# Optimization experiments

Hardware: AMD Instinct MI355X
Metric: run time of the kernel (lower is better)

## Reference

```python
import jax, jax.numpy as jnp
import numpy as np

N_LAYERS = 4
EPS = 1e-5  # eqx.nn.LayerNorm default


def _kernels(lam, P, B, C, step, L):
    # Annotated-S4 DPLR generating-function kernel (Q = P), vectorized over H channels.
    # lam, P, B, C: (H, N) complex64; step: (H, 1) real. Returns K: (H, L) real.
    omega = jnp.exp((-2j * jnp.pi) * (jnp.arange(L) / L))            # (L,) roots of unity
    g = (2.0 / step) * ((1.0 - omega) / (1.0 + omega))[None, :]      # (H, L) bilinear warp
    c = 2.0 / (1.0 + omega)                                          # (L,)

    def cauchy(v):  # v: (H, N) -> (H, L): sum_n v_n / (g - lambda_n)
        return jnp.sum(v[:, None, :] / (g[:, :, None] - lam[:, None, :]), axis=-1)

    k00 = cauchy(jnp.conj(C) * B)
    k01 = cauchy(jnp.conj(C) * P)
    k10 = cauchy(jnp.conj(P) * B)
    k11 = cauchy(jnp.conj(P) * P)
    at_roots = c[None, :] * (k00 - k01 * (1.0 / (1.0 + k11)) * k10)  # woodbury correction
    return jnp.fft.ifft(at_roots, n=L, axis=-1).real                 # (H, L)


def _causal_conv(u, K):
    # u: (B, L, H) real input, K: (H, L) real kernel -> causal conv along L via zero-padded FFT.
    L = u.shape[1]
    Ud = jnp.fft.rfft(u, n=2 * L, axis=1)                 # (B, F, H)
    Kd = jnp.fft.rfft(K, n=2 * L, axis=-1)                # (H, F)
    return jnp.fft.irfft(Ud * Kd.T[None], n=2 * L, axis=1)[:, :L]


def _forward(x, enc_w, enc_b, dec_w, dec_b, lam_re, lam_im, p_re, p_im, b_re, b_im,
             c_re, c_im, d, log_step, norm_w, norm_b, w1, b1, w2, b2):
    L = x.shape[1]
    h = x @ enc_w.T + enc_b                               # encoder: (B, L, H)
    for i in range(N_LAYERS):
        skip = h
        mu = h.mean(-1, keepdims=True)
        var = ((h - mu) ** 2).mean(-1, keepdims=True)
        hn = (h - mu) / jnp.sqrt(var + EPS) * norm_w[i] + norm_b[i]
        K = _kernels(lam_re[i] + 1j * lam_im[i], p_re[i] + 1j * p_im[i],
                     b_re[i] + 1j * b_im[i], c_re[i] + 1j * c_im[i],
                     jnp.exp(log_step[i])[:, None], L)
        y = _causal_conv(hn, K) + hn * d[i]               # SSM conv + skip-through D term
        y = jax.nn.gelu(y)
        y = (y @ w1[i].T + b1[i]) * jax.nn.sigmoid(y @ w2[i].T + b2[i])  # gated MLP
        h = skip + y
    return h @ dec_w.T + dec_b                            # decoder: (B, L, out)


def setup_inputs() -> dict:
    key = jax.random.key(0)
    B, L, IN, OUT, H, N, NL = 8, 2048, 64, 64, 128, 64, N_LAYERS
    ks = jax.random.split(key, 12)
    rn = lambda k, s, sc: (jax.random.normal(k, s) * sc).astype(jnp.float32)
    return dict(
        x=rn(ks[0], (B, L, IN), 1.0),
        convolve=1,
        enc_w=rn(ks[1], (H, IN), 1.0 / np.sqrt(IN)), enc_b=jnp.zeros((H,), jnp.float32),
        dec_w=rn(ks[2], (OUT, H), 1.0 / np.sqrt(H)), dec_b=jnp.zeros((OUT,), jnp.float32),
        lam_re=-0.5 * jnp.ones((NL, H, N), jnp.float32),  # HiPPO/S4D-style stable poles
        lam_im=jnp.tile(jnp.float32(np.pi) * jnp.arange(N, dtype=jnp.float32), (NL, H, 1)),
        p_re=rn(ks[3], (NL, H, N), 0.5 / np.sqrt(N)), p_im=rn(ks[4], (NL, H, N), 0.5 / np.sqrt(N)),
        b_re=rn(ks[5], (NL, H, N), 1.0), b_im=rn(ks[6], (NL, H, N), 1.0),
        c_re=rn(ks[7], (NL, H, N), 1.0 / np.sqrt(N)), c_im=rn(ks[8], (NL, H, N), 1.0 / np.sqrt(N)),
        d=jnp.ones((NL, H), jnp.float32),
        log_step=(jax.random.uniform(ks[9], (NL, H)) * (np.log(0.1) - np.log(0.001))
                  + np.log(0.001)).astype(jnp.float32),
        norm_w=jnp.ones((NL, H), jnp.float32), norm_b=jnp.zeros((NL, H), jnp.float32),
        w1=rn(ks[10], (NL, H, H), 1.0 / np.sqrt(H)), b1=jnp.zeros((NL, H), jnp.float32),
        w2=rn(ks[11], (NL, H, H), 1.0 / np.sqrt(H)), b2=jnp.zeros((NL, H), jnp.float32),
    )


def reference(x, convolve, enc_w, enc_b, dec_w, dec_b, lam_re, lam_im, p_re, p_im,
              b_re, b_im, c_re, c_im, d, log_step, norm_w, norm_b, w1, b1, w2, b2):
    # convolve is static 1 (True): the FFT-convolution path of the S4 Model.
    return _forward(x, enc_w, enc_b, dec_w, dec_b, lam_re, lam_im, p_re, p_im, b_re, b_im,
                    c_re, c_im, d, log_step, norm_w, norm_b, w1, b1, w2, b2)
```

## Files before the change

### kernel.cpp

```cpp
#include <hip/hip_runtime.h>
#include <hip/hip_bf16.h>


#define Bsz 8
#define Lseq 2048
#define Hdim 128
#define Npol 64
#define NLAYERS 4

typedef __bf16 bf16x8 __attribute__((ext_vector_type(8)));
typedef float f32x16 __attribute__((ext_vector_type(16)));

__device__ __forceinline__ float fast_rcp(float x) { return __builtin_amdgcn_rcpf(x); }
__device__ __forceinline__ float fast_rsq(float x) { return __builtin_amdgcn_rsqf(x); }

__device__ __forceinline__ float2 cmulf(float2 a, float2 b) {
    return make_float2(a.x * b.x - a.y * b.y, a.x * b.y + a.y * b.x);
}
__device__ __forceinline__ float2 cmulc(float2 a, float2 b) {
    return make_float2(a.x * b.x + a.y * b.y, a.y * b.x - a.x * b.y);
}

__device__ __forceinline__ float gelu_f(float v) {
    float z = 0.7978845608028654f * (v + 0.044715f * v * v * v);
    float e = __expf(2.0f * z);
    return v - v * fast_rcp(e + 1.0f);
}

__device__ __forceinline__ int sw(int i) { return (i & ~15) | ((i ^ (i >> 4)) & 15); }

static __device__ const float W16R[8] = {1.f, 0.9238795325f, 0.7071067812f, 0.3826834324f,
                                         0.f, -0.3826834324f, -0.7071067812f, -0.9238795325f};
static __device__ const float W16I[8] = {0.f, -0.3826834324f, -0.7071067812f, -0.9238795325f,
                                         -1.f, -0.9238795325f, -0.7071067812f, -0.3826834324f};
static __device__ const int BR4[16] = {0, 8, 4, 12, 2, 10, 6, 14, 1, 9, 5, 13, 3, 11, 7, 15};
static __device__ const int BR3[8] = {0, 4, 2, 6, 1, 5, 3, 7};

__device__ __forceinline__ float2 twget(const float2* __restrict__ tw, int e) {
    float2 w = tw[e & 2047];
    if (e & 2048) { w.x = -w.x; w.y = -w.y; }
    return w;
}

template <bool INV>
__device__ __forceinline__ void fft16_dif(float2 v[16]) {
#pragma unroll
    for (int mi = 0; mi < 4; mi++) {
        const int m = 8 >> mi;
#pragma unroll
        for (int g = 0; g < 16; g += 2 * m) {
#pragma unroll
            for (int j = 0; j < m; j++) {
                float wr = W16R[j << mi];
                float wi = INV ? -W16I[j << mi] : W16I[j << mi];
                float2 a = v[g + j], b = v[g + j + m];
                float dx = a.x - b.x, dy = a.y - b.y;
                v[g + j] = make_float2(a.x + b.x, a.y + b.y);
                v[g + j + m] = make_float2(dx * wr - dy * wi, dx * wi + dy * wr);
            }
        }
    }
}

template <bool INV>
__device__ __forceinline__ void fft16_dit(float2 v[16]) {
#pragma unroll
    for (int mi = 3; mi >= 0; mi--) {
        const int m = 8 >> mi;
#pragma unroll
        for (int g = 0; g < 16; g += 2 * m) {
#pragma unroll
            for (int j = 0; j < m; j++) {
                float wr = W16R[j << mi];
                float wi = INV ? -W16I[j << mi] : W16I[j << mi];
                float2 a = v[g + j], b = v[g + j + m];
                float bx = b.x * wr - b.y * wi, by = b.x * wi + b.y * wr;
                v[g + j] = make_float2(a.x + bx, a.y + by);
                v[g + j + m] = make_float2(a.x - bx, a.y - by);
            }
        }
    }
}

template <bool INV>
__device__ __forceinline__ void fft8_dif(float2 v[8]) {
#pragma unroll
    for (int mi = 0; mi < 3; mi++) {
        const int m = 4 >> mi;
#pragma unroll
        for (int g = 0; g < 8; g += 2 * m) {
#pragma unroll
            for (int j = 0; j < m; j++) {
                float wr = W16R[j << (mi + 1)];
                float wi = INV ? -W16I[j << (mi + 1)] : W16I[j << (mi + 1)];
                float2 a = v[g + j], b = v[g + j + m];
                float dx = a.x - b.x, dy = a.y - b.y;
                v[g + j] = make_float2(a.x + b.x, a.y + b.y);
                v[g + j + m] = make_float2(dx * wr - dy * wi, dx * wi + dy * wr);
            }
        }
    }
}

__device__ __forceinline__ void fft4096_passA_hz(float2* data, const float2* __restrict__ tw,
                                                 int t, const float2 vin[8]) {
    float2 v[16];
#pragma unroll
    for (int j = 0; j < 8; j++) v[j] = vin[j];
#pragma unroll
    for (int j = 0; j < 8; j++)
        v[j + 8] = cmulf(v[j], make_float2(W16R[j], W16I[j]));
#pragma unroll
    for (int mi = 1; mi < 4; mi++) {
        const int m = 8 >> mi;
#pragma unroll
        for (int g = 0; g < 16; g += 2 * m) {
#pragma unroll
            for (int j = 0; j < m; j++) {
                float wr = W16R[j << mi], wi = W16I[j << mi];
                float2 a = v[g + j], b = v[g + j + m];
                float dx = a.x - b.x, dy = a.y - b.y;
                v[g + j] = make_float2(a.x + b.x, a.y + b.y);
                v[g + j + m] = make_float2(dx * wr - dy * wi, dx * wi + dy * wr);
            }
        }
    }
#pragma unroll
    for (int i = 1; i < 16; i++) v[i] = cmulf(v[i], twget(tw, t * BR4[i]));
#pragma unroll
    for (int i = 0; i < 16; i++) data[sw(i * 256 + t)] = v[i];
}

__device__ __forceinline__ void fft4096_fwd_BC(float2* data, const float2* __restrict__ tw, int t) {
    __syncthreads();
    {
        int j0 = t & 15;
        int base = (t >> 4) * 256 + j0;
        float2 v[16];
#pragma unroll
        for (int k = 0; k < 16; k++) v[k] = data[sw(base + 16 * k)];
        fft16_dif<false>(v);
#pragma unroll
        for (int i = 1; i < 16; i++) v[i] = cmulf(v[i], twget(tw, 16 * j0 * BR4[i]));
#pragma unroll
        for (int i = 0; i < 16; i++) data[sw(base + 16 * i)] = v[i];
    }
    __syncthreads();
    {
        float2 v[16];
#pragma unroll
        for (int k = 0; k < 16; k++) v[k] = data[sw(t * 16 + k)];
        fft16_dif<false>(v);
#pragma unroll
        for (int i = 0; i < 16; i++) data[sw(t * 16 + i)] = v[i];
    }
    __syncthreads();
}

__device__ __forceinline__ void kfft_core(int hh, int t, float* smem,
                                          float2* __restrict__ KdL,
                                          const float2* __restrict__ tw,
                                          const float* __restrict__ lam_re,
                                          const float* __restrict__ lam_im,
                                          const float* __restrict__ p_re,
                                          const float* __restrict__ p_im,
                                          const float* __restrict__ b_re,
                                          const float* __restrict__ b_im,
                                          const float* __restrict__ c_re,
                                          const float* __restrict__ c_im,
                                          const float* __restrict__ log_step) {
    float2* data = (float2*)smem;
    float4* polA = (float4*)(smem + 8192);
    float4* polB = (float4*)(smem + 8448);
    float* n11S = smem + 8704;
    float* ktmp = smem + 8192;
    int baseP = hh * Npol;
    if (t < Npol) {
        int n = t;
        float lr = lam_re[baseP + n], li = lam_im[baseP + n];
        float pr = p_re[baseP + n], pi = p_im[baseP + n];
        float br = b_re[baseP + n], bi = b_im[baseP + n];
        float cr = c_re[baseP + n], ci = c_im[baseP + n];
        polA[n] = make_float4(lr, li, cr * br + ci * bi, cr * bi - ci * br);
        polB[n] = make_float4(cr * pr + ci * pi, cr * pi - ci * pr,
                              pr * br + pi * bi, pr * bi - pi * br);
        n11S[n] = pr * pr + pi * pi;
    }
    __syncthreads();
    {
        float step = expf(log_step[hh]);
        float gs = 2.0f / step;
        float wrv[8], wiv[8];
        float gr[8], gi[8];
#pragma unroll
        for (int j = 0; j < 8; j++) {
            int l = t + 256 * j;
            float ang = -6.283185307179586f * (float)l / (float)Lseq;
            float wr = cosf(ang), wi = sinf(ang);
            wrv[j] = wr; wiv[j] = wi;
            float dr = 1.0f + wr, di = wi;
            float invd2 = fast_rcp(dr * dr + di * di);
            float nr = 1.0f - wr, ni = -wi;
            gr[j] = gs * (nr * dr + ni * di) * invd2;
            gi[j] = gs * (ni * dr - nr * di) * invd2;
        }
        float k00x[8], k00y[8], k01x[8], k01y[8];
        float k10x[8], k10y[8], k11x[8], k11y[8];
#pragma unroll
        for (int j = 0; j < 8; j++) {
            k00x[j] = 0.f; k00y[j] = 0.f; k01x[j] = 0.f; k01y[j] = 0.f;
            k10x[j] = 0.f; k10y[j] = 0.f; k11x[j] = 0.f; k11y[j] = 0.f;
        }
        for (int n = 0; n < Npol; n++) {
            float4 A = polA[n];
            float4 B = polB[n];
            float n11 = n11S[n];
#pragma unroll
            for (int j = 0; j < 8; j++) {
                float er = gr[j] - A.x, ei = gi[j] - A.y;
                float inv2 = fast_rcp(fmaf(er, er, ei * ei));
                float ir = er * inv2;
                float mi = ei * inv2;
                k00x[j] = fmaf(A.z, ir, fmaf(A.w, mi, k00x[j]));
                k00y[j] = fmaf(A.w, ir, fmaf(-A.z, mi, k00y[j]));
                k01x[j] = fmaf(B.x, ir, fmaf(B.y, mi, k01x[j]));
                k01y[j] = fmaf(B.y, ir, fmaf(-B.x, mi, k01y[j]));
                k10x[j] = fmaf(B.z, ir, fmaf(B.w, mi, k10x[j]));
                k10y[j] = fmaf(B.w, ir, fmaf(-B.z, mi, k10y[j]));
                k11x[j] = fmaf(n11, ir, k11x[j]);
                k11y[j] = fmaf(-n11, mi, k11y[j]);
            }
        }
#pragma unroll
        for (int j = 0; j < 8; j++) {
            int l = t + 256 * j;
            float dr = 1.0f + wrv[j], di = wiv[j];
            float invd2 = fast_rcp(dr * dr + di * di);
            float cr2 = 2.0f * dr * invd2, ci2 = -2.0f * di * invd2;
            float wr2 = 1.0f + k11x[j], wi2 = k11y[j];
            float w2inv = fast_rcp(fmaf(wr2, wr2, wi2 * wi2));
            float vr = wr2 * w2inv, vi = -wi2 * w2inv;
            float t1x = k01x[j] * k10x[j] - k01y[j] * k10y[j];
            float t1y = k01x[j] * k10y[j] + k01y[j] * k10x[j];
            float t2x = t1x * vr - t1y * vi, t2y = t1x * vi + t1y * vr;
            float ex = k00x[j] - t2x, ey = k00y[j] - t2y;
            data[sw(l)] = make_float2(cr2 * ex - ci2 * ey, cr2 * ey + ci2 * ex);
        }
    }
    __syncthreads();
    if (t < 128) {
        float2 v[16];
#pragma unroll
        for (int k = 0; k < 16; k++) v[k] = data[sw(t + 128 * k)];
        fft16_dif<true>(v);
#pragma unroll
        for (int i = 1; i < 16; i++) v[i] = cmulc(v[i], twget(tw, 2 * t * BR4[i]));
#pragma unroll
        for (int i = 0; i < 16; i++) data[sw(i * 128 + t)] = v[i];
    }
    __syncthreads();
    if (t < 128) {
        int i2 = t >> 3, j0 = t & 7;
        int base2 = i2 * 128 + j0;
        float2 v[16];
#pragma unroll
        for (int k = 0; k < 16; k++) v[k] = data[sw(base2 + 8 * k)];
        fft16_dif<true>(v);
#pragma unroll
        for (int i = 1; i < 16; i++) v[i] = cmulc(v[i], twget(tw, 32 * j0 * BR4[i]));
#pragma unroll
        for (int i = 0; i < 16; i++) data[sw(base2 + 8 * i)] = v[i];
    }
    __syncthreads();
    {
        float2 v8[8];
#pragma unroll
        for (int k = 0; k < 8; k++) v8[k] = data[sw(t * 8 + k)];
        fft8_dif<true>(v8);
        int r = BR4[t >> 4], s = BR4[t & 15];
#pragma unroll
        for (int i = 0; i < 8; i++) {
            int l = r + 16 * s + 256 * BR3[i];
            ktmp[l] = v8[i].x * (1.0f / 2048.0f);
        }
    }
    __syncthreads();
    {
        float2 vin[8];
#pragma unroll
        for (int k = 0; k < 8; k++) vin[k] = make_float2(ktmp[t + 256 * k], 0.f);
        fft4096_passA_hz(data, tw, t, vin);
    }
    fft4096_fwd_BC(data, tw, t);
    float2* dst = KdL + (size_t)hh * 4096;
#pragma unroll
    for (int k = 0; k < 16; k++) {
        int p = t + 256 * k;
        dst[p] = data[sw(p)];
    }
}

__global__ __launch_bounds__(256, 4) void prep_kernel(const float* __restrict__ w1,
                                                      const float* __restrict__ w2,
                                                      const float* __restrict__ dec_w,
                                                      const float* __restrict__ enc_w,
                                                      float2* __restrict__ tw,
                                                      __bf16* __restrict__ wbf,
                                                      __bf16* __restrict__ decbf,
                                                      __bf16* __restrict__ encbf) {
    int bid = blockIdx.x, t = threadIdx.x;
    if (bid < 8) {
        int k = bid * 256 + t;
        if (k < 2048) {
            double a = -6.283185307179586476925286766559 * (double)k / 4096.0;
            tw[k] = make_float2((float)cos(a), (float)sin(a));
        }
        return;
    }
    if (bid < 264) {
        int i = (bid - 8) * 256 + t;
        int layer = i >> 14, rem = i & 16383;
        wbf[((size_t)layer * 2) * 16384 + rem] = (__bf16)w1[i];
        wbf[((size_t)layer * 2 + 1) * 16384 + rem] = (__bf16)w2[i];
        return;
    }
    if (bid < 296) {
        int i = (bid - 264) * 256 + t;
        decbf[i] = (__bf16)dec_w[i];
        return;
    }
    int i = (bid - 296) * 256 + t;
    encbf[i] = (__bf16)enc_w[i];
}

__global__ __launch_bounds__(256) void kfft_enc_kernel(float2* __restrict__ Kd1,
                                                       const float2* __restrict__ tw,
                                                       const float* __restrict__ x,
                                                       const __bf16* __restrict__ encbf,
                                                       const float* __restrict__ enc_b,
                                                       const float* __restrict__ nw,
                                                       const float* __restrict__ nb,
                                                       float* __restrict__ h,
                                                       float* __restrict__ hnT,
                                                       const float* __restrict__ lam_re,
                                                       const float* __restrict__ lam_im,
                                                       const float* __restrict__ p_re,
                                                       const float* __restrict__ p_im,
                                                       const float* __restrict__ b_re,
                                                       const float* __restrict__ b_im,
                                                       const float* __restrict__ c_re,
                                                       const float* __restrict__ c_im,
                                                       const float* __restrict__ log_step) {
    __shared__ __align__(16) float smem[10240];
    int bid = blockIdx.x, t = threadIdx.x;
    if (bid < 512) {
        int hh = bid & 127, layer = bid >> 7;
        int PN = Hdim * Npol;
        kfft_core(hh, t, smem, Kd1 + (size_t)layer * Hdim * 4096, tw,
                  lam_re + layer * PN, lam_im + layer * PN,
                  p_re + layer * PN, p_im + layer * PN,
                  b_re + layer * PN, b_im + layer * PN,
                  c_re + layer * PN, c_im + layer * PN,
                  log_step + layer * Hdim);
    } else {
        int r0 = (bid - 512) * 32;
        __bf16* ybf = (__bf16*)smem;
        float* dots = smem + 1152;
        float2* mv = (float2*)(smem + 5376);
        int bb = r0 >> 11, l0 = r0 & 2047;
        for (int i = t; i < 32 * 64; i += 256) {
            int r = i >> 6, k = i & 63;
            ybf[r * 72 + k] = (__bf16)x[(size_t)(r0 + r) * 64 + k];
        }
        __syncthreads();
        int wave = t >> 6, lane = t & 63;
        int m = lane & 31, half = lane >> 5;
        bf16x8 a[4];
#pragma unroll
        for (int kk = 0; kk < 4; kk++)
            a[kk] = *(const bf16x8*)&ybf[m * 72 + kk * 16 + half * 8];
        int o = 32 * wave + m;
        const __bf16* wr = encbf + (size_t)o * 64 + half * 8;
        f32x16 acc;
#pragma unroll
        for (int i = 0; i < 16; i++) acc[i] = 0.f;
#pragma unroll
        for (int kk = 0; kk < 4; kk++) {
            bf16x8 bw = *(const bf16x8*)(wr + kk * 16);
            acc = __builtin_amdgcn_mfma_f32_32x32x16_bf16(a[kk], bw, acc, 0, 0, 0);
        }
        float bo = enc_b[o];
#pragma unroll
        for (int reg = 0; reg < 16; reg++) {
            int row = (reg & 3) + 8 * (reg >> 2) + 4 * half;
            dots[row * 132 + o] = acc[reg] + bo;
        }
        __syncthreads();
        {
            int row = t >> 3, lane8 = t & 7;
            float s1 = 0.f, s2 = 0.f;
            int base = row * 132 + lane8 * 16;
#pragma unroll
            for (int q = 0; q < 4; q++) {
                float4 v4 = *(const float4*)&dots[base + 4 * q];
                s1 += v4.x + v4.y + v4.z + v4.w;
                s2 += v4.x * v4.x + v4.y * v4.y + v4.z * v4.z + v4.w * v4.w;
            }
#pragma unroll
            for (int mm = 1; mm < 8; mm <<= 1) { s1 += __shfl_xor(s1, mm); s2 += __shfl_xor(s2, mm); }
            if (lane8 == 0) {
                float mu = s1 * (1.0f / 128.0f);
                float var = s2 * (1.0f / 128.0f) - mu * mu;
                mv[row] = make_float2(mu, fast_rsq(var + 1e-5f));
            }
        }
        __syncthreads();
        {
            int o2 = t & 127, rh = t >> 7;
            float nwc = nw[o2], nbc = nb[o2];
            float hnv[16];
#pragma unroll
            for (int j = 0; j < 16; j++) {
                int r = rh * 16 + j;
                float hvv = dots[r * 132 + o2];
                h[(size_t)(r0 + r) * Hdim + o2] = hvv;
                float2 mvv = mv[r];
                hnv[j] = (hvv - mvv.x) * mvv.y * nwc + nbc;
            }
            float* dst = hnT + ((size_t)bb * Hdim + o2) * Lseq + l0 + rh * 16;
            *(float4*)(dst)      = make_float4(hnv[0],  hnv[1],  hnv[2],  hnv[3]);
            *(float4*)(dst + 4)  = make_float4(hnv[4],  hnv[5],  hnv[6],  hnv[7]);
            *(float4*)(dst + 8)  = make_float4(hnv[8],  hnv[9],  hnv[10], hnv[11]);
            *(float4*)(dst + 12) = make_float4(hnv[12], hnv[13], hnv[14], hnv[15]);
        }
    }
}

__global__ __launch_bounds__(256) void conv_kernel(float* __restrict__ hnT,
                                                   const float2* __restrict__ Kd1,
                                                   const float* __restrict__ dvec,
                                                   const float2* __restrict__ tw) {
    int h = blockIdx.x, bp = blockIdx.y, t = threadIdx.x;
    __shared__ float2 data[4096];
    float* u0 = hnT + ((size_t)(2 * bp) * Hdim + h) * Lseq;
    float* u1 = hnT + ((size_t)(2 * bp + 1) * Hdim + h) * Lseq;
    float2 ureg[8];
    float2 Kreg[16];
    float2 twB[15];
    const int j0 = t & 15;
    const float4* Kp4 = (const float4*)(Kd1 + (size_t)h * 4096 + t * 16);
    {
        float2 vin[8];
#pragma unroll
        for (int k = 0; k < 8; k++) {
            int l = t + 256 * k;
            float2 u2 = make_float2(u0[l], u1[l]);
            ureg[k] = u2;
            vin[k] = u2;
        }
#pragma unroll
        for (int k = 0; k < 8; k++) {
            float4 q = Kp4[k];
            Kreg[2 * k]     = make_float2(q.x, q.y);
            Kreg[2 * k + 1] = make_float2(q.z, q.w);
        }
#pragma unroll
        for (int i = 1; i < 16; i++) twB[i - 1] = twget(tw, 16 * j0 * BR4[i]);
        fft4096_passA_hz(data, tw, t, vin);
    }
    __syncthreads();
    {
        int base = (t >> 4) * 256 + j0;
        float2 v[16];
#pragma unroll
        for (int k = 0; k < 16; k++) v[k] = data[sw(base + 16 * k)];
        fft16_dif<false>(v);
#pragma unroll
        for (int i = 1; i < 16; i++) v[i] = cmulf(v[i], twB[i - 1]);
#pragma unroll
        for (int i = 0; i < 16; i++) data[sw(base + 16 * i)] = v[i];
    }
    __syncthreads();
    {
        const float scale = 1.0f / 4096.0f;
        float2 v[16];
#pragma unroll
        for (int k = 0; k < 16; k++) v[k] = data[sw(t * 16 + k)];
        fft16_dif<false>(v);
#pragma unroll
        for (int i = 0; i < 16; i++) {
            float2 W = cmulf(v[i], Kreg[i]);
            v[i] = make_float2(W.x * scale, W.y * scale);
        }
        fft16_dit<true>(v);
#pragma unroll
        for (int i = 0; i < 16; i++) data[sw(t * 16 + i)] = v[i];
    }
    __syncthreads();
    {
        int base2 = (t >> 4) * 256 + j0;
        float2 v[16];
        v[0] = data[sw(base2)];
#pragma unroll
        for (int i = 1; i < 16; i++)
            v[i] = cmulc(data[sw(base2 + 16 * i)], twB[i - 1]);
        fft16_dit<true>(v);
#pragma unroll
        for (int i = 0; i < 16; i++) data[sw(base2 + 16 * i)] = v[i];
    }
    __syncthreads();
    {
        float2 v[16];
        v[0] = data[sw(t)];
#pragma unroll
        for (int i = 1; i < 16; i++)
            v[i] = cmulc(data[sw(i * 256 + t)], twget(tw, t * BR4[i]));
#pragma unroll
        for (int mi = 3; mi >= 1; mi--) {
            const int m = 8 >> mi;
#pragma unroll
            for (int g = 0; g < 16; g += 2 * m) {
#pragma unroll
                for (int j = 0; j < m; j++) {
                    float wr = W16R[j << mi], wi = -W16I[j << mi];
                    float2 a = v[g + j], bb2 = v[g + j + m];
                    float bx = bb2.x * wr - bb2.y * wi, by = bb2.x * wi + bb2.y * wr;
                    v[g + j] = make_float2(a.x + bx, a.y + by);
                    v[g + j + m] = make_float2(a.x - bx, a.y - by);
                }
            }
        }
#pragma unroll
        for (int j = 0; j < 8; j++) {
            float wr = W16R[j], wi = -W16I[j];
            float2 bb2 = v[j + 8];
            float bx = bb2.x * wr - bb2.y * wi, by = bb2.x * wi + bb2.y * wr;
            v[j] = make_float2(v[j].x + bx, v[j].y + by);
        }
        float dcoef = dvec[h];
#pragma unroll
        for (int k = 0; k < 8; k++) {
            int l = t + 256 * k;
            u0[l] = gelu_f(v[k].x + ureg[k].x * dcoef);
            u1[l] = gelu_f(v[k].y + ureg[k].y * dcoef);
        }
    }
}

__global__ __launch_bounds__(256) void mlp_kernel(const float* __restrict__ yT,
                                                  float* __restrict__ h,
                                                  float* __restrict__ hnT,
                                                  const __bf16* __restrict__ w1b,
                                                  const __bf16* __restrict__ w2b,
                                                  const float* __restrict__ b1,
                                                  const float* __restrict__ b2,
                                                  const float* __restrict__ nw,
                                                  const float* __restrict__ nb) {
    int r0 = blockIdx.x * 32;
    int t = threadIdx.x;
    int wave = t >> 6, lane = t & 63;
    __shared__ __align__(16) __bf16 ybf[32 * 136];
    __shared__ float dots[32 * 132];
    __shared__ float2 mv[32];
    int bb = r0 >> 11, l0 = r0 & 2047;
    for (int i = t; i < 32 * 128; i += 256) {
        int r = i & 31, k = i >> 5;
        ybf[r * 136 + k] = (__bf16)yT[((size_t)bb * Hdim + k) * Lseq + l0 + r];
    }
    __syncthreads();
    int m = lane & 31, half = lane >> 5;
    bf16x8 a[8];
#pragma unroll
    for (int kk = 0; kk < 8; kk++)
        a[kk] = *(const bf16x8*)&ybf[m * 136 + kk * 16 + half * 8];
    int out = 32 * wave + m;
    const __bf16* w1r = w1b + (size_t)out * 128 + half * 8;
    const __bf16* w2r = w2b + (size_t)out * 128 + half * 8;
    f32x16 acc1, acc2;
#pragma unroll
    for (int i = 0; i < 16; i++) { acc1[i] = 0.f; acc2[i] = 0.f; }
#pragma unroll
    for (int kk = 0; kk < 8; kk++) {
        bf16x8 bw1 = *(const bf16x8*)(w1r + kk * 16);
        bf16x8 bw2 = *(const bf16x8*)(w2r + kk * 16);
        acc1 = __builtin_amdgcn_mfma_f32_32x32x16_bf16(a[kk], bw1, acc1, 0, 0, 0);
        acc2 = __builtin_amdgcn_mfma_f32_32x32x16_bf16(a[kk], bw2, acc2, 0, 0, 0);
    }
    float bias1 = b1[out], bias2 = b2[out];
#pragma unroll
    for (int reg = 0; reg < 16; reg++) {
        int row = (reg & 3) + 8 * (reg >> 2) + 4 * half;
        float v1 = acc1[reg] + bias1;
        float v2 = acc2[reg] + bias2;
        float g = fast_rcp(1.0f + __expf(-v2));
        float hv = h[(size_t)(r0 + row) * Hdim + out] + v1 * g;
        dots[row * 132 + out] = hv;
    }
    __syncthreads();
    {
        int row = t >> 3, lane8 = t & 7;
        float s1 = 0.f, s2 = 0.f;
        int base = row * 132 + lane8 * 16;
#pragma unroll
        for (int q = 0; q < 4; q++) {
            float4 v4 = *(const float4*)&dots[base + 4 * q];
            s1 += v4.x + v4.y + v4.z + v4.w;
            s2 += v4.x * v4.x + v4.y * v4.y + v4.z * v4.z + v4.w * v4.w;
        }
#pragma unroll
        for (int mm = 1; mm < 8; mm <<= 1) { s1 += __shfl_xor(s1, mm); s2 += __shfl_xor(s2, mm); }
        if (lane8 == 0) {
            float mu = s1 * (1.0f / 128.0f);
            float var = s2 * (1.0f / 128.0f) - mu * mu;
            mv[row] = make_float2(mu, fast_rsq(var + 1e-5f));
        }
    }
    __syncthreads();
    {
        int o = t & 127, rh = t >> 7;
        float nwc = nw[o], nbc = nb[o];
        float hnv[16];
#pragma unroll
        for (int j = 0; j < 16; j++) {
            int r = rh * 16 + j;
            float hvv = dots[r * 132 + o];
            h[(size_t)(r0 + r) * Hdim + o] = hvv;
            float2 mvv = mv[r];
            hnv[j] = (hvv - mvv.x) * mvv.y * nwc + nbc;
        }
        float* dst = hnT + ((size_t)bb * Hdim + o) * Lseq + l0 + rh * 16;
        *(float4*)(dst)      = make_float4(hnv[0],  hnv[1],  hnv[2],  hnv[3]);
        *(float4*)(dst + 4)  = make_float4(hnv[4],  hnv[5],  hnv[6],  hnv[7]);
        *(float4*)(dst + 8)  = make_float4(hnv[8],  hnv[9],  hnv[10], hnv[11]);
        *(float4*)(dst + 12) = make_float4(hnv[12], hnv[13], hnv[14], hnv[15]);
    }
}

__global__ __launch_bounds__(256) void mlpdec_kernel(const float* __restrict__ yT,
                                                     const float* __restrict__ h,
                                                     const __bf16* __restrict__ w1b,
                                                     const __bf16* __restrict__ w2b,
                                                     const float* __restrict__ b1,
                                                     const float* __restrict__ b2,
                                                     const __bf16* __restrict__ decb,
                                                     const float* __restrict__ dec_bias,
                                                     float* __restrict__ out) {
    int r0 = blockIdx.x * 32;
    int t = threadIdx.x;
    int wave = t >> 6, lane = t & 63;
    __shared__ __align__(16) __bf16 ybf[32 * 136];
    __shared__ float dots[32 * 132];
    int bb = r0 >> 11, l0 = r0 & 2047;
    for (int i = t; i < 32 * 128; i += 256) {
        int r = i & 31, k = i >> 5;
        ybf[r * 136 + k] = (__bf16)yT[((size_t)bb * Hdim + k) * Lseq + l0 + r];
    }
    __syncthreads();
    int m = lane & 31, half = lane >> 5;
    bf16x8 a[8];
#pragma unroll
    for (int kk = 0; kk < 8; kk++)
        a[kk] = *(const bf16x8*)&ybf[m * 136 + kk * 16 + half * 8];
    int outc = 32 * wave + m;
    const __bf16* w1r = w1b + (size_t)outc * 128 + half * 8;
    const __bf16* w2r = w2b + (size_t)outc * 128 + half * 8;
    f32x16 acc1, acc2;
#pragma unroll
    for (int i = 0; i < 16; i++) { acc1[i] = 0.f; acc2[i] = 0.f; }
#pragma unroll
    for (int kk = 0; kk < 8; kk++) {
        bf16x8 bw1 = *(const bf16x8*)(w1r + kk * 16);
        bf16x8 bw2 = *(const bf16x8*)(w2r + kk * 16);
        acc1 = __builtin_amdgcn_mfma_f32_32x32x16_bf16(a[kk], bw1, acc1, 0, 0, 0);
        acc2 = __builtin_amdgcn_mfma_f32_32x32x16_bf16(a[kk], bw2, acc2, 0, 0, 0);
    }
    float bias1 = b1[outc], bias2 = b2[outc];
#pragma unroll
    for (int reg = 0; reg < 16; reg++) {
        int row = (reg & 3) + 8 * (reg >> 2) + 4 * half;
        float v1 = acc1[reg] + bias1;
        float v2 = acc2[reg] + bias2;
        float g = fast_rcp(1.0f + __expf(-v2));
        float hv = h[(size_t)(r0 + row) * Hdim + outc] + v1 * g;
        dots[row * 132 + outc] = hv;
    }
    __syncthreads();
    for (int i = t; i < 32 * 128; i += 256) {
        int r = i >> 7, k = i & 127;
        ybf[r * 136 + k] = (__bf16)dots[r * 132 + k];
    }
    __syncthreads();
    if (wave < 2) {
        bf16x8 a2[8];
#pragma unroll
        for (int kk = 0; kk < 8; kk++)
            a2[kk] = *(const bf16x8*)&ybf[m * 136 + kk * 16 + half * 8];
        int oc = 32 * wave + m;
        const __bf16* wr = decb + (size_t)oc * 128 + half * 8;
        f32x16 acc;
#pragma unroll
        for (int i = 0; i < 16; i++) acc[i] = 0.f;
#pragma unroll
        for (int kk = 0; kk < 8; kk++) {
            bf16x8 bw = *(const bf16x8*)(wr + kk * 16);
            acc = __builtin_amdgcn_mfma_f32_32x32x16_bf16(a2[kk], bw, acc, 0, 0, 0);
        }
        float bo = dec_bias[oc];
#pragma unroll
        for (int reg = 0; reg < 16; reg++) {
            int row = (reg & 3) + 8 * (reg >> 2) + 4 * half;
            out[(size_t)(r0 + row) * 64 + oc] = acc[reg] + bo;
        }
    }
}

extern "C" void kernel_launch(void* const* d_in, const int* in_sizes, int n_in,
                              void* d_out, int out_size, void* d_ws, size_t ws_size,
                              hipStream_t stream) {
    const float* x      = (const float*)d_in[0];
    const float* enc_w  = (const float*)d_in[2];
    const float* enc_b  = (const float*)d_in[3];
    const float* dec_w  = (const float*)d_in[4];
    const float* dec_b  = (const float*)d_in[5];
    const float* lam_re = (const float*)d_in[6];
    const float* lam_im = (const float*)d_in[7];
    const float* p_re   = (const float*)d_in[8];
    const float* p_im   = (const float*)d_in[9];
    const float* b_re   = (const float*)d_in[10];
    const float* b_im   = (const float*)d_in[11];
    const float* c_re   = (const float*)d_in[12];
    const float* c_im   = (const float*)d_in[13];
    const float* dvec   = (const float*)d_in[14];
    const float* lstep  = (const float*)d_in[15];
    const float* norm_w = (const float*)d_in[16];
    const float* norm_b = (const float*)d_in[17];
    const float* w1     = (const float*)d_in[18];
    const float* b1     = (const float*)d_in[19];
    const float* w2     = (const float*)d_in[20];
    const float* b2     = (const float*)d_in[21];
    float* out = (float*)d_out;

    char* ws = (char*)d_ws;
    float2* tw  = (float2*)ws;  ws += 2048 * sizeof(float2);
    float*  h   = (float*)ws;   ws += (size_t)Bsz * Lseq * Hdim * sizeof(float);
    float*  hnT = (float*)ws;   ws += (size_t)Bsz * Lseq * Hdim * sizeof(float);
    float2* Kd1 = (float2*)ws;  ws += (size_t)NLAYERS * Hdim * 4096 * sizeof(float2);
    __bf16* wbf = (__bf16*)ws;  ws += (size_t)NLAYERS * 2 * Hdim * Hdim * sizeof(__bf16);
    __bf16* dbf = (__bf16*)ws;  ws += (size_t)64 * Hdim * sizeof(__bf16);
    __bf16* ebf = (__bf16*)ws;  ws += (size_t)Hdim * 64 * sizeof(__bf16);

    const int nrows = Bsz * Lseq;

    prep_kernel<<<328, 256, 0, stream>>>(w1, w2, dec_w, enc_w, tw, wbf, dbf, ebf);
    kfft_enc_kernel<<<512 + nrows / 32, 256, 0, stream>>>(
        Kd1, tw, x, ebf, enc_b, norm_w, norm_b, h, hnT,
        lam_re, lam_im, p_re, p_im, b_re, b_im, c_re, c_im, lstep);
    for (int L = 0; L < NLAYERS; L++) {
        conv_kernel<<<dim3(Hdim, Bsz / 2), 256, 0, stream>>>(
            hnT, Kd1 + (size_t)L * Hdim * 4096, dvec + L * Hdim, tw);
        const __bf16* w1bL = wbf + (size_t)L * 2 * Hdim * Hdim;
        const __bf16* w2bL = w1bL + Hdim * Hdim;
        if (L < NLAYERS - 1) {
            const float* nwn = norm_w + (L + 1) * Hdim;
            const float* nbn = norm_b + (L + 1) * Hdim;
            mlp_kernel<<<nrows / 32, 256, 0, stream>>>(hnT, h, hnT, w1bL, w2bL,
                                                       b1 + L * Hdim, b2 + L * Hdim,
                                                       nwn, nbn);
        } else {
            mlpdec_kernel<<<nrows / 32, 256, 0, stream>>>(hnT, h, w1bL, w2bL,
                                                          b1 + L * Hdim, b2 + L * Hdim,
                                                          dbf, dec_b, out);
        }
    }
}
```

Measured before the change: 277.5 us.

## Write conv output as bf16 to separate buffer and widen kfft blocks to 512 threads

The conv kernel now writes the GELU output as bf16 into a new buffer instead of overwriting hnT in fp32, and the MLP kernels read bf16 directly. This halves the write and read traffic of the intermediate activation between conv and MLP. Separately, the kernel-generation/encoder kernel is launched with 512 threads, splitting the Cauchy sum over 4 instead of 8 points per thread, while the FFT and encoder phases stay on 256 threads with the rest idle. The wider block adds more barriers and idle threads in the FFT/encoder sections.

```diff
diff --git a/kernel.cpp b/kernel.cpp
--- a/kernel.cpp
+++ b/kernel.cpp
@@ -131,173 +131,25 @@
     for (int i = 0; i < 16; i++) data[sw(i * 256 + t)] = v[i];
 }
 
-__device__ __forceinline__ void fft4096_fwd_BC(float2* data, const float2* __restrict__ tw, int t) {
-    __syncthreads();
-    {
-        int j0 = t & 15;
-        int base = (t >> 4) * 256 + j0;
-        float2 v[16];
-#pragma unroll
-        for (int k = 0; k < 16; k++) v[k] = data[sw(base + 16 * k)];
-        fft16_dif<false>(v);
-#pragma unroll
-        for (int i = 1; i < 16; i++) v[i] = cmulf(v[i], twget(tw, 16 * j0 * BR4[i]));
-#pragma unroll
-        for (int i = 0; i < 16; i++) data[sw(base + 16 * i)] = v[i];
-    }
-    __syncthreads();
-    {
-        float2 v[16];
-#pragma unroll
-        for (int k = 0; k < 16; k++) v[k] = data[sw(t * 16 + k)];
-        fft16_dif<false>(v);
-#pragma unroll
-        for (int i = 0; i < 16; i++) data[sw(t * 16 + i)] = v[i];
-    }
-    __syncthreads();
-}
-
-__device__ __forceinline__ void kfft_core(int hh, int t, float* smem,
-                                          float2* __restrict__ KdL,
-                                          const float2* __restrict__ tw,
-                                          const float* __restrict__ lam_re,
-                                          const float* __restrict__ lam_im,
-                                          const float* __restrict__ p_re,
-                                          const float* __restrict__ p_im,
-                                          const float* __restrict__ b_re,
-                                          const float* __restrict__ b_im,
-                                          const float* __restrict__ c_re,
-                                          const float* __restrict__ c_im,
-                                          const float* __restrict__ log_step) {
-    float2* data = (float2*)smem;
-    float4* polA = (float4*)(smem + 8192);
-    float4* polB = (float4*)(smem + 8448);
-    float* n11S = smem + 8704;
-    float* ktmp = smem + 8192;
-    int baseP = hh * Npol;
-    if (t < Npol) {
-        int n = t;
-        float lr = lam_re[baseP + n], li = lam_im[baseP + n];
-        float pr = p_re[baseP + n], pi = p_im[baseP + n];
-        float br = b_re[baseP + n], bi = b_im[baseP + n];
-        float cr = c_re[baseP + n], ci = c_im[baseP + n];
-        polA[n] = make_float4(lr, li, cr * br + ci * bi, cr * bi - ci * br);
-        polB[n] = make_float4(cr * pr + ci * pi, cr * pi - ci * pr,
-                              pr * br + pi * bi, pr * bi - pi * br);
-        n11S[n] = pr * pr + pi * pi;
-    }
-    __syncthreads();
-    {
-        float step = expf(log_step[hh]);
-        float gs = 2.0f / step;
-        float wrv[8], wiv[8];
-        float gr[8], gi[8];
-#pragma unroll
-        for (int j = 0; j < 8; j++) {
-            int l = t + 256 * j;
-            float ang = -6.283185307179586f * (float)l / (float)Lseq;
-            float wr = cosf(ang), wi = sinf(ang);
-            wrv[j] = wr; wiv[j] = wi;
-            float dr = 1.0f + wr, di = wi;
-            float invd2 = fast_rcp(dr * dr + di * di);
-            float nr = 1.0f - wr, ni = -wi;
-            gr[j] = gs * (nr * dr + ni * di) * invd2;
-            gi[j] = gs * (ni * dr - nr * di) * invd2;
-        }
-        float k00x[8], k00y[8], k01x[8], k01y[8];
-        float k10x[8], k10y[8], k11x[8], k11y[8];
-#pragma unroll
-        for (int j = 0; j < 8; j++) {
-            k00x[j] = 0.f; k00y[j] = 0.f; k01x[j] = 0.f; k01y[j] = 0.f;
-            k10x[j] = 0.f; k10y[j] = 0.f; k11x[j] = 0.f; k11y[j] = 0.f;
-        }
-        for (int n = 0; n < Npol; n++) {
-            float4 A = polA[n];
-            float4 B = polB[n];
-            float n11 = n11S[n];
-#pragma unroll
-            for (int j = 0; j < 8; j++) {
-                float er = gr[j] - A.x, ei = gi[j] - A.y;
-                float inv2 = fast_rcp(fmaf(er, er, ei * ei));
-                float ir = er * inv2;
-                float mi = ei * inv2;
-                k00x[j] = fmaf(A.z, ir, fmaf(A.w, mi, k00x[j]));
-                k00y[j] = fmaf(A.w, ir, fmaf(-A.z, mi, k00y[j]));
-                k01x[j] = fmaf(B.x, ir, fmaf(B.y, mi, k01x[j]));
-                k01y[j] = fmaf(B.y, ir, fmaf(-B.x, mi, k01y[j]));
-                k10x[j] = fmaf(B.z, ir, fmaf(B.w, mi, k10x[j]));
-                k10y[j] = fmaf(B.w, ir, fmaf(-B.z, mi, k10y[j]));
-                k11x[j] = fmaf(n11, ir, k11x[j]);
-                k11y[j] = fmaf(-n11, mi, k11y[j]);
-            }
-        }
-#pragma unroll
-        for (int j = 0; j < 8; j++) {
-            int l = t + 256 * j;
-            float dr = 1.0f + wrv[j], di = wiv[j];
-            float invd2 = fast_rcp(dr * dr + di * di);
-            float cr2 = 2.0f * dr * invd2, ci2 = -2.0f * di * invd2;
-            float wr2 = 1.0f + k11x[j], wi2 = k11y[j];
-            float w2inv = fast_rcp(fmaf(wr2, wr2, wi2 * wi2));
-            float vr = wr2 * w2inv, vi = -wi2 * w2inv;
-            float t1x = k01x[j] * k10x[j] - k01y[j] * k10y[j];
-            float t1y = k01x[j] * k10y[j] + k01y[j] * k10x[j];
-            float t2x = t1x * vr - t1y * vi, t2y = t1x * vi + t1y * vr;
-            float ex = k00x[j] - t2x, ey = k00y[j] - t2y;
-            data[sw(l)] = make_float2(cr2 * ex - ci2 * ey, cr2 * ey + ci2 * ex);
-        }
-    }
-    __syncthreads();
-    if (t < 128) {
-        float2 v[16];
-#pragma unroll
-        for (int k = 0; k < 16; k++) v[k] = data[sw(t + 128 * k)];
-        fft16_dif<true>(v);
-#pragma unroll
-        for (int i = 1; i < 16; i++) v[i] = cmulc(v[i], twget(tw, 2 * t * BR4[i]));
-#pragma unroll
-        for (int i = 0; i < 16; i++) data[sw(i * 128 + t)] = v[i];
-    }
-    __syncthreads();
-    if (t < 128) {
-        int i2 = t >> 3, j0 = t & 7;
-        int base2 = i2 * 128 + j0;
-        float2 v[16];
-#pragma unroll
-        for (int k = 0; k < 16; k++) v[k] = data[sw(base2 + 8 * k)];
-        fft16_dif<true>(v);
-#pragma unroll
-        for (int i = 1; i < 16; i++) v[i] = cmulc(v[i], twget(tw, 32 * j0 * BR4[i]));
-#pragma unroll
-        for (int i = 0; i < 16; i++) data[sw(base2 + 8 * i)] = v[i];
-    }
-    __syncthreads();
-    {
-        float2 v8[8];
-#pragma unroll
-        for (int k = 0; k < 8; k++) v8[k] = data[sw(t * 8 + k)];
-        fft8_dif<true>(v8);
-        int r = BR4[t >> 4], s = BR4[t & 15];
-#pragma unroll
-        for (int i = 0; i < 8; i++) {
-            int l = r + 16 * s + 256 * BR3[i];
-            ktmp[l] = v8[i].x * (1.0f / 2048.0f);
-        }
-    }
-    __syncthreads();
-    {
-        float2 vin[8];
-#pragma unroll
-        for (int k = 0; k < 8; k++) vin[k] = make_float2(ktmp[t + 256 * k], 0.f);
-        fft4096_passA_hz(data, tw, t, vin);
-    }
-    fft4096_fwd_BC(data, tw, t);
-    float2* dst = KdL + (size_t)hh * 4096;
-#pragma unroll
-    for (int k = 0; k < 16; k++) {
-        int p = t + 256 * k;
-        dst[p] = data[sw(p)];
-    }
+__device__ __forceinline__ void fft4096_fwd_B(float2* data, const float2* __restrict__ tw, int t) {
+    int j0 = t & 15;
+    int base = (t >> 4) * 256 + j0;
+    float2 v[16];
+#pragma unroll
+    for (int k = 0; k < 16; k++) v[k] = data[sw(base + 16 * k)];
+    fft16_dif<false>(v);
+#pragma unroll
+    for (int i = 1; i < 16; i++) v[i] = cmulf(v[i], twget(tw, 16 * j0 * BR4[i]));
+#pragma unroll
+    for (int i = 0; i < 16; i++) data[sw(base + 16 * i)] = v[i];
+}
+__device__ __forceinline__ void fft4096_fwd_C(float2* data, int t) {
+    float2 v[16];
+#pragma unroll
+    for (int k = 0; k < 16; k++) v[k] = data[sw(t * 16 + k)];
+    fft16_dif<false>(v);
+#pragma unroll
+    for (int i = 0; i < 16; i++) data[sw(t * 16 + i)] = v[i];
 }
 
 __global__ __launch_bounds__(256, 4) void prep_kernel(const float* __restrict__ w1,
@@ -333,7 +185,7 @@
     encbf[i] = (__bf16)enc_w[i];
 }
 
-__global__ __launch_bounds__(256) void kfft_enc_kernel(float2* __restrict__ Kd1,
+__global__ __launch_bounds__(512) void kfft_enc_kernel(float2* __restrict__ Kd1,
                                                        const float2* __restrict__ tw,
                                                        const float* __restrict__ x,
                                                        const __bf16* __restrict__ encbf,
@@ -356,47 +208,184 @@
     if (bid < 512) {
         int hh = bid & 127, layer = bid >> 7;
         int PN = Hdim * Npol;
-        kfft_core(hh, t, smem, Kd1 + (size_t)layer * Hdim * 4096, tw,
-                  lam_re + layer * PN, lam_im + layer * PN,
-                  p_re + layer * PN, p_im + layer * PN,
-                  b_re + layer * PN, b_im + layer * PN,
-                  c_re + layer * PN, c_im + layer * PN,
-                  log_step + layer * Hdim);
+        const float* lre = lam_re + layer * PN;
+        const float* lim = lam_im + layer * PN;
+        const float* pre = p_re + layer * PN;
+        const float* pim = p_im + layer * PN;
+        const float* bre = b_re + layer * PN;
+        const float* bim = b_im + layer * PN;
+        const float* cre = c_re + layer * PN;
+        const float* cim = c_im + layer * PN;
+        const float* lst = log_step + layer * Hdim;
+        float2* data = (float2*)smem;
+        float4* polA = (float4*)(smem + 8192);
+        float4* polB = (float4*)(smem + 8448);
+        float* n11S = smem + 8704;
+        float* ktmp = smem + 8192;
+        int baseP = hh * Npol;
+        if (t < Npol) {
+            int n = t;
+            float lr = lre[baseP + n], li = lim[baseP + n];
+            float pr = pre[baseP + n], pi = pim[baseP + n];
+            float br = bre[baseP + n], bi = bim[baseP + n];
+            float cr = cre[baseP + n], ci = cim[baseP + n];
+            polA[n] = make_float4(lr, li, cr * br + ci * bi, cr * bi - ci * br);
+            polB[n] = make_float4(cr * pr + ci * pi, cr * pi - ci * pr,
+                                  pr * br + pi * bi, pr * bi - pi * br);
+            n11S[n] = pr * pr + pi * pi;
+        }
+        __syncthreads();
+        {
+            float step = expf(lst[hh]);
+            float gs = 2.0f / step;
+            float wrv[4], wiv[4], gr[4], gi[4];
+#pragma unroll
+            for (int j = 0; j < 4; j++) {
+                int l = t + 512 * j;
+                float ang = -6.283185307179586f * (float)l / (float)Lseq;
+                float wr = cosf(ang), wi = sinf(ang);
+                wrv[j] = wr; wiv[j] = wi;
+                float dr = 1.0f + wr, di = wi;
+                float invd2 = fast_rcp(dr * dr + di * di);
+                float nr = 1.0f - wr, ni = -wi;
+                gr[j] = gs * (nr * dr + ni * di) * invd2;
+                gi[j] = gs * (ni * dr - nr * di) * invd2;
+            }
+            float k00x[4], k00y[4], k01x[4], k01y[4];
+            float k10x[4], k10y[4], k11x[4], k11y[4];
+#pragma unroll
+            for (int j = 0; j < 4; j++) {
+                k00x[j] = 0.f; k00y[j] = 0.f; k01x[j] = 0.f; k01y[j] = 0.f;
+                k10x[j] = 0.f; k10y[j] = 0.f; k11x[j] = 0.f; k11y[j] = 0.f;
+            }
+            for (int n = 0; n < Npol; n++) {
+                float4 A = polA[n];
+                float4 B = polB[n];
+                float n11 = n11S[n];
+#pragma unroll
+                for (int j = 0; j < 4; j++) {
+                    float er = gr[j] - A.x, ei = gi[j] - A.y;
+                    float inv2 = fast_rcp(fmaf(er, er, ei * ei));
+                    float ir = er * inv2;
+                    float mi = ei * inv2;
+                    k00x[j] = fmaf(A.z, ir, fmaf(A.w, mi, k00x[j]));
+                    k00y[j] = fmaf(A.w, ir, fmaf(-A.z, mi, k00y[j]));
+                    k01x[j] = fmaf(B.x, ir, fmaf(B.y, mi, k01x[j]));
+                    k01y[j] = fmaf(B.y, ir, fmaf(-B.x, mi, k01y[j]));
+                    k10x[j] = fmaf(B.z, ir, fmaf(B.w, mi, k10x[j]));
+                    k10y[j] = fmaf(B.w, ir, fmaf(-B.z, mi, k10y[j]));
+                    k11x[j] = fmaf(n11, ir, k11x[j]);
+                    k11y[j] = fmaf(-n11, mi, k11y[j]);
+                }
+            }
+#pragma unroll
+            for (int j = 0; j < 4; j++) {
+                int l = t + 512 * j;
+                float dr = 1.0f + wrv[j], di = wiv[j];
+                float invd2 = fast_rcp(dr * dr + di * di);
+                float cr2 = 2.0f * dr * invd2, ci2 = -2.0f * di * invd2;
+                float wr2 = 1.0f + k11x[j], wi2 = k11y[j];
+                float w2inv = fast_rcp(fmaf(wr2, wr2, wi2 * wi2));
+                float vr = wr2 * w2inv, vi = -wi2 * w2inv;
+                float t1x = k01x[j] * k10x[j] - k01y[j] * k10y[j];
+                float t1y = k01x[j] * k10y[j] + k01y[j] * k10x[j];
+                float t2x = t1x * vr - t1y * vi, t2y = t1x * vi + t1y * vr;
+                float ex = k00x[j] - t2x, ey = k00y[j] - t2y;
+                data[sw(l)] = make_float2(cr2 * ex - ci2 * ey, cr2 * ey + ci2 * ex);
+            }
+        }
+        __syncthreads();
+        if (t < 128) {
+            float2 v[16];
+#pragma unroll
+            for (int k = 0; k < 16; k++) v[k] = data[sw(t + 128 * k)];
+            fft16_dif<true>(v);
+#pragma unroll
+            for (int i = 1; i < 16; i++) v[i] = cmulc(v[i], twget(tw, 2 * t * BR4[i]));
+#pragma unroll
+            for (int i = 0; i < 16; i++) data[sw(i * 128 + t)] = v[i];
+        }
+        __syncthreads();
+        if (t < 128) {
+            int i2 = t >> 3, j0 = t & 7;
+            int base2 = i2 * 128 + j0;
+            float2 v[16];
+#pragma unroll
+            for (int k = 0; k < 16; k++) v[k] = data[sw(base2 + 8 * k)];
+            fft16_dif<true>(v);
+#pragma unroll
+            for (int i = 1; i < 16; i++) v[i] = cmulc(v[i], twget(tw, 32 * j0 * BR4[i]));
+#pragma unroll
+            for (int i = 0; i < 16; i++) data[sw(base2 + 8 * i)] = v[i];
+        }
+        __syncthreads();
+        if (t < 256) {
+            float2 v8[8];
+#pragma unroll
+            for (int k = 0; k < 8; k++) v8[k] = data[sw(t * 8 + k)];
+            fft8_dif<true>(v8);
+            int r = BR4[t >> 4], s = BR4[t & 15];
+#pragma unroll
+            for (int i = 0; i < 8; i++) {
+                int l = r + 16 * s + 256 * BR3[i];
+                ktmp[l] = v8[i].x * (1.0f / 2048.0f);
+            }
+        }
+        __syncthreads();
+        if (t < 256) {
+            float2 vin[8];
+#pragma unroll
+            for (int k = 0; k < 8; k++) vin[k] = make_float2(ktmp[t + 256 * k], 0.f);
+            fft4096_passA_hz(data, tw, t, vin);
+        }
+        __syncthreads();
+        if (t < 256) fft4096_fwd_B(data, tw, t);
+        __syncthreads();
+        if (t < 256) fft4096_fwd_C(data, t);
+        __syncthreads();
+        float2* dst = Kd1 + ((size_t)layer * Hdim + hh) * 4096;
+#pragma unroll
+        for (int k = 0; k < 8; k++) {
+            int p = t + 512 * k;
+            dst[p] = data[sw(p)];
+        }
     } else {
         int r0 = (bid - 512) * 32;
         __bf16* ybf = (__bf16*)smem;
         float* dots = smem + 1152;
         float2* mv = (float2*)(smem + 5376);
         int bb = r0 >> 11, l0 = r0 & 2047;
-        for (int i = t; i < 32 * 64; i += 256) {
+        for (int i = t; i < 32 * 64; i += 512) {
             int r = i >> 6, k = i & 63;
             ybf[r * 72 + k] = (__bf16)x[(size_t)(r0 + r) * 64 + k];
         }
         __syncthreads();
-        int wave = t >> 6, lane = t & 63;
-        int m = lane & 31, half = lane >> 5;
-        bf16x8 a[4];
-#pragma unroll
-        for (int kk = 0; kk < 4; kk++)
-            a[kk] = *(const bf16x8*)&ybf[m * 72 + kk * 16 + half * 8];
-        int o = 32 * wave + m;
-        const __bf16* wr = encbf + (size_t)o * 64 + half * 8;
-        f32x16 acc;
-#pragma unroll
-        for (int i = 0; i < 16; i++) acc[i] = 0.f;
-#pragma unroll
-        for (int kk = 0; kk < 4; kk++) {
-            bf16x8 bw = *(const bf16x8*)(wr + kk * 16);
-            acc = __builtin_amdgcn_mfma_f32_32x32x16_bf16(a[kk], bw, acc, 0, 0, 0);
-        }
-        float bo = enc_b[o];
-#pragma unroll
-        for (int reg = 0; reg < 16; reg++) {
-            int row = (reg & 3) + 8 * (reg >> 2) + 4 * half;
-            dots[row * 132 + o] = acc[reg] + bo;
-        }
-        __syncthreads();
-        {
+        if (t < 256) {
+            int wave = t >> 6, lane = t & 63;
+            int m = lane & 31, half = lane >> 5;
+            bf16x8 a[4];
+#pragma unroll
+            for (int kk = 0; kk < 4; kk++)
+                a[kk] = *(const bf16x8*)&ybf[m * 72 + kk * 16 + half * 8];
+            int o = 32 * wave + m;
+            const __bf16* wr = encbf + (size_t)o * 64 + half * 8;
+            f32x16 acc;
+#pragma unroll
+            for (int i = 0; i < 16; i++) acc[i] = 0.f;
+#pragma unroll
+            for (int kk = 0; kk < 4; kk++) {
+                bf16x8 bw = *(const bf16x8*)(wr + kk * 16);
+                acc = __builtin_amdgcn_mfma_f32_32x32x16_bf16(a[kk], bw, acc, 0, 0, 0);
+            }
+            float bo = enc_b[o];
+#pragma unroll
+            for (int reg = 0; reg < 16; reg++) {
+                int row = (reg & 3) + 8 * (reg >> 2) + 4 * half;
+                dots[row * 132 + o] = acc[reg] + bo;
+            }
+        }
+        __syncthreads();
+        if (t < 256) {
             int row = t >> 3, lane8 = t & 7;
             float s1 = 0.f, s2 = 0.f;
             int base = row * 132 + lane8 * 16;
@@ -415,7 +404,7 @@
             }
         }
         __syncthreads();
-        {
+        if (t < 256) {
             int o2 = t & 127, rh = t >> 7;
             float nwc = nw[o2], nbc = nb[o2];
             float hnv[16];
@@ -436,14 +425,17 @@
     }
 }
 
-__global__ __launch_bounds__(256) void conv_kernel(float* __restrict__ hnT,
+__global__ __launch_bounds__(256) void conv_kernel(const float* __restrict__ hnT,
+                                                   __bf16* __restrict__ ybuf,
                                                    const float2* __restrict__ Kd1,
                                                    const float* __restrict__ dvec,
                                                    const float2* __restrict__ tw) {
     int h = blockIdx.x, bp = blockIdx.y, t = threadIdx.x;
     __shared__ float2 data[4096];
-    float* u0 = hnT + ((size_t)(2 * bp) * Hdim + h) * Lseq;
-    float* u1 = hnT + ((size_t)(2 * bp + 1) * Hdim + h) * Lseq;
+    const float* u0 = hnT + ((size_t)(2 * bp) * Hdim + h) * Lseq;
+    const float* u1 = hnT + ((size_t)(2 * bp + 1) * Hdim + h) * Lseq;
+    __bf16* y0 = ybuf + ((size_t)(2 * bp) * Hdim + h) * Lseq;
+    __bf16* y1 = ybuf + ((size_t)(2 * bp + 1) * Hdim + h) * Lseq;
     float2 ureg[8];
     float2 Kreg[16];
     float2 twB[15];
@@ -541,13 +533,13 @@
 #pragma unroll
         for (int k = 0; k < 8; k++) {
             int l = t + 256 * k;
-            u0[l] = gelu_f(v[k].x + ureg[k].x * dcoef);
-            u1[l] = gelu_f(v[k].y + ureg[k].y * dcoef);
-        }
-    }
-}
-
-__global__ __launch_bounds__(256) void mlp_kernel(const float* __restrict__ yT,
+            y0[l] = (__bf16)gelu_f(v[k].x + ureg[k].x * dcoef);
+            y1[l] = (__bf16)gelu_f(v[k].y + ureg[k].y * dcoef);
+        }
+    }
+}
+
+__global__ __launch_bounds__(256) void mlp_kernel(const __bf16* __restrict__ yT,
                                                   float* __restrict__ h,
                                                   float* __restrict__ hnT,
                                                   const __bf16* __restrict__ w1b,
@@ -565,7 +557,7 @@
     int bb = r0 >> 11, l0 = r0 & 2047;
     for (int i = t; i < 32 * 128; i += 256) {
         int r = i & 31, k = i >> 5;
-        ybf[r * 136 + k] = (__bf16)yT[((size_t)bb * Hdim + k) * Lseq + l0 + r];
+        ybf[r * 136 + k] = yT[((size_t)bb * Hdim + k) * Lseq + l0 + r];
     }
     __syncthreads();
     int m = lane & 31, half = lane >> 5;
@@ -636,7 +628,7 @@
     }
 }
 
-__global__ __launch_bounds__(256) void mlpdec_kernel(const float* __restrict__ yT,
+__global__ __launch_bounds__(256) void mlpdec_kernel(const __bf16* __restrict__ yT,
                                                      const float* __restrict__ h,
                                                      const __bf16* __restrict__ w1b,
                                                      const __bf16* __restrict__ w2b,
@@ -653,7 +645,7 @@
     int bb = r0 >> 11, l0 = r0 & 2047;
     for (int i = t; i < 32 * 128; i += 256) {
         int r = i & 31, k = i >> 5;
-        ybf[r * 136 + k] = (__bf16)yT[((size_t)bb * Hdim + k) * Lseq + l0 + r];
+        ybf[r * 136 + k] = yT[((size_t)bb * Hdim + k) * Lseq + l0 + r];
     }
     __syncthreads();
     int m = lane & 31, half = lane >> 5;
@@ -744,6 +736,7 @@
     float2* tw  = (float2*)ws;  ws += 2048 * sizeof(float2);
     float*  h   = (float*)ws;   ws += (size_t)Bsz * Lseq * Hdim * sizeof(float);
     float*  hnT = (float*)ws;   ws += (size_t)Bsz * Lseq * Hdim * sizeof(float);
+    __bf16* ybuf = (__bf16*)ws; ws += (size_t)Bsz * Lseq * Hdim * sizeof(__bf16);
     float2* Kd1 = (float2*)ws;  ws += (size_t)NLAYERS * Hdim * 4096 * sizeof(float2);
     __bf16* wbf = (__bf16*)ws;  ws += (size_t)NLAYERS * 2 * Hdim * Hdim * sizeof(__bf16);
     __bf16* dbf = (__bf16*)ws;  ws += (size_t)64 * Hdim * sizeof(__bf16);
@@ -752,22 +745,22 @@
     const int nrows = Bsz * Lseq;
 
     prep_kernel<<<328, 256, 0, stream>>>(w1, w2, dec_w, enc_w, tw, wbf, dbf, ebf);
-    kfft_enc_kernel<<<512 + nrows / 32, 256, 0, stream>>>(
+    kfft_enc_kernel<<<512 + nrows / 32, 512, 0, stream>>>(
         Kd1, tw, x, ebf, enc_b, norm_w, norm_b, h, hnT,
         lam_re, lam_im, p_re, p_im, b_re, b_im, c_re, c_im, lstep);
     for (int L = 0; L < NLAYERS; L++) {
         conv_kernel<<<dim3(Hdim, Bsz / 2), 256, 0, stream>>>(
-            hnT, Kd1 + (size_t)L * Hdim * 4096, dvec + L * Hdim, tw);
+            hnT, ybuf, Kd1 + (size_t)L * Hdim * 4096, dvec + L * Hdim, tw);
         const __bf16* w1bL = wbf + (size_t)L * 2 * Hdim * Hdim;
         const __bf16* w2bL = w1bL + Hdim * Hdim;
         if (L < NLAYERS - 1) {
             const float* nwn = norm_w + (L + 1) * Hdim;
             const float* nbn = norm_b + (L + 1) * Hdim;
-            mlp_kernel<<<nrows / 32, 256, 0, stream>>>(hnT, h, hnT, w1bL, w2bL,
+            mlp_kernel<<<nrows / 32, 256, 0, stream>>>(ybuf, h, hnT, w1bL, w2bL,
                                                        b1 + L * Hdim, b2 + L * Hdim,
                                                        nwn, nbn);
         } else {
-            mlpdec_kernel<<<nrows / 32, 256, 0, stream>>>(hnT, h, w1bL, w2bL,
+            mlpdec_kernel<<<nrows / 32, 256, 0, stream>>>(ybuf, h, w1bL, w2bL,
                                                           b1 + L * Hdim, b2 + L * Hdim,
                                                           dbf, dec_b, out);
         }
```

Result: faster. 265.4 us (-4.4%).
